# Optimization experiments

Hardware: AMD Instinct MI355X
Metric: run time of the kernel (lower is better)

The kernel has to match this reference:

```python
import jax, jax.numpy as jnp
import numpy as np

NUM_FIELDS = 40
EMBED_DIM = 64
ATTN_DIM = 32

def _triu_index(n):
    i, j = np.triu_indices(n, k=1)
    return jnp.asarray(i, jnp.int32), jnp.asarray(j, jnp.int32)

def setup_inputs() -> dict:
    key = jax.random.key(0)
    k0, k1, k2, k3, k4, k5 = jax.random.split(key, 6)
    B = 8192
    inputs = jax.random.normal(k0, (B, NUM_FIELDS, EMBED_DIM), dtype=jnp.float32)
    # attention MLP params (PyTorch Linear default init scale ~ 1/sqrt(fan_in))
    s1 = 1.0 / np.sqrt(EMBED_DIM)
    s2 = 1.0 / np.sqrt(ATTN_DIM)
    W1 = jax.random.uniform(k1, (EMBED_DIM, ATTN_DIM), jnp.float32, -s1, s1)
    b1 = jax.random.uniform(k2, (ATTN_DIM,), jnp.float32, -s1, s1)
    w2 = jax.random.uniform(k3, (ATTN_DIM,), jnp.float32, -s2, s2)
    p = jax.random.uniform(k4, (EMBED_DIM,), jnp.float32, -s1, s1)
    return {"inputs": inputs, "W1": W1, "b1": b1, "w2": w2, "p": p}

def reference(inputs, W1, b1, w2, p):
    idx0, idx1 = _triu_index(NUM_FIELDS)  # [P], P = 780 pairs
    # gather pairwise field embeddings and take elementwise product: [B, P, D]
    prod = inputs[:, idx0, :] * inputs[:, idx1, :]
    # tiny attention MLP: Linear -> ReLU -> Linear(no bias) -> softmax over pairs
    h = jax.nn.relu(jnp.einsum('bpd,da->bpa', prod, W1) + b1)  # [B, P, A]
    logits = jnp.einsum('bpa,a->bp', h, w2)                    # [B, P]
    attn = jax.nn.softmax(logits, axis=1)                      # softmax over pair dim
    # attention-weighted sum pooling over pairs: [B, D]
    pooled = jnp.einsum('bp,bpd->bd', attn, prod)
    # final linear projection to scalar (dropout=0 / eval -> identity)
    return jnp.einsum('bd,d->b', pooled, p)
```

## Files before the change

### kernel.cpp

```cpp
#include <hip/hip_runtime.h>


typedef _Float16 f16;
typedef f16 f16x2 __attribute__((ext_vector_type(2)));
typedef f16 f16x4 __attribute__((ext_vector_type(4)));
typedef f16 f16x8 __attribute__((ext_vector_type(8)));
typedef float fx16 __attribute__((ext_vector_type(16)));

#define NF 40
#define NB 8192
#define STR 88

union V8 { f16x8 v8; f16x4 v4[2]; f16x2 v2[4]; };

__global__ __launch_bounds__(256, 4) void afm_kernel(
    const float* __restrict__ x,
    const float* __restrict__ W1,
    const float* __restrict__ b1,
    const float* __restrict__ w2,
    const float* __restrict__ p,
    float* __restrict__ out)
{
    __shared__ __align__(16) f16 xh[4][NF * STR];

    const int tid  = threadIdx.x;
    const int wid  = tid >> 6;
    const int lane = tid & 63;
    const int b    = blockIdx.x * 4 + wid;

    f16* Xs = &xh[wid][0];

    const float4* xb = (const float4*)(x + (size_t)b * (NF * 64));
#pragma unroll
    for (int t = 0; t < 5; ++t) {
        int g = t * 64 + lane;
        float4 v0 = xb[g * 2];
        float4 v1 = xb[g * 2 + 1];
        V8 w;
        w.v4[0] = f16x4{ (f16)v0.x, (f16)v0.y, (f16)v0.z, (f16)v0.w };
        w.v4[1] = f16x4{ (f16)v1.x, (f16)v1.y, (f16)v1.z, (f16)v1.w };
        int row = g >> 3, gg = g & 7;
        *(f16x8*)(Xs + row * STR + gg * 8) = w.v8;
    }

    const int nl = lane & 31;
    const int hh = lane >> 5;
    const int h8 = hh * 8;

    f16x8 w1f[4];
#pragma unroll
    for (int kt = 0; kt < 4; ++kt)
#pragma unroll
        for (int j = 0; j < 8; ++j)
            w1f[kt][j] = (f16)W1[(kt * 16 + h8 + j) * 32 + nl];

    f16x2 pp[16];
#pragma unroll
    for (int kt = 0; kt < 4; ++kt)
#pragma unroll
        for (int m = 0; m < 4; ++m) {
            f16x2 t2 = { (f16)p[kt * 16 + h8 + 2 * m], (f16)p[kt * 16 + h8 + 2 * m + 1] };
            pp[kt * 4 + m] = t2;
        }

    fx16 b1C;
    f16x2 w2h[8];
#pragma unroll
    for (int r = 0; r < 16; ++r) {
        int a = (r & 3) + 8 * (r >> 2) + 4 * hh;
        b1C[r] = b1[a];
    }
#pragma unroll
    for (int m = 0; m < 8; ++m) {
        int r = 2 * m;
        int a = (r & 3) + 8 * (r >> 2) + 4 * hh;
        f16x2 t2 = { (f16)(w2[a] * 1.44269504f), (f16)(w2[a + 1] * 1.44269504f) };
        w2h[m] = t2;
    }

    f16x8 xif8[4];
    {
        const f16* src = Xs + nl * STR + h8;
#pragma unroll
        for (int kt = 0; kt < 4; ++kt)
            xif8[kt] = *(const f16x8*)(src + kt * 16);
    }

    float accW = 0.f, accWS = 0.f;

    auto body = [&](const f16x8* xi, int jrow, bool valid) {
        const f16* base = Xs + jrow * STR + h8;
        V8 pr[4];
#pragma unroll
        for (int kt = 0; kt < 4; ++kt) {
            f16x8 xj = *(const f16x8*)(base + kt * 16);
            pr[kt].v8 = xi[kt] * xj;
        }
        fx16 C = __builtin_amdgcn_mfma_f32_32x32x16_f16(w1f[0], pr[0].v8, b1C, 0, 0, 0);
        C = __builtin_amdgcn_mfma_f32_32x32x16_f16(w1f[1], pr[1].v8, C, 0, 0, 0);
        C = __builtin_amdgcn_mfma_f32_32x32x16_f16(w1f[2], pr[2].v8, C, 0, 0, 0);
        C = __builtin_amdgcn_mfma_f32_32x32x16_f16(w1f[3], pr[3].v8, C, 0, 0, 0);
        float s0 = 0.f, s1 = 0.f, s2 = 0.f, s3 = 0.f;
#pragma unroll
        for (int m = 0; m < 4; ++m) {
            s0 = __builtin_amdgcn_fdot2(pr[0].v2[m], pp[m],      s0, false);
            s1 = __builtin_amdgcn_fdot2(pr[1].v2[m], pp[4 + m],  s1, false);
            s2 = __builtin_amdgcn_fdot2(pr[2].v2[m], pp[8 + m],  s2, false);
            s3 = __builtin_amdgcn_fdot2(pr[3].v2[m], pp[12 + m], s3, false);
        }
        float sp = (s0 + s1) + (s2 + s3);
        const f16x2 z2 = { (f16)0.f, (f16)0.f };
        float l0 = 0.f, l1 = 0.f;
#pragma unroll
        for (int m = 0; m < 8; ++m) {
            f16x2 hm = __builtin_bit_cast(f16x2,
                __builtin_amdgcn_cvt_pkrtz(C[2 * m], C[2 * m + 1]));
            hm = __builtin_elementwise_max(hm, z2);
            if (m & 1) l1 = __builtin_amdgcn_fdot2(hm, w2h[m], l1, false);
            else       l0 = __builtin_amdgcn_fdot2(hm, w2h[m], l0, false);
        }
        float l = l0 + l1;
        l += __shfl_xor(l, 32);
        float w = __builtin_amdgcn_exp2f(l);
        if (!valid) w = 0.f;
        accW += w;
        accWS = fmaf(w, sp, accWS);
    };

    for (int t = 1; t <= 24; ++t) {
        int jrow = (t <= 16) ? ((nl + t) & 31) : (t + 15);
        bool valid = (t != 16) || (nl < 16);
        body(xif8, jrow, valid);
    }
    {
        int q = nl < 28 ? nl : 27;
        float disc = 225.0f - 8.0f * (float)q;
        int ii = (int)((15.0f - sqrtf(disc)) * 0.5f);
        if (ii * (15 - ii) / 2 > q) --ii;
        if ((ii + 1) * (14 - ii) / 2 <= q) ++ii;
        int jj = q - ii * (15 - ii) / 2 + ii + 1;
        int iC = 32 + ii, jC = 32 + jj;
        f16x8 xi2[4];
        const f16* src = Xs + iC * STR + h8;
#pragma unroll
        for (int kt = 0; kt < 4; ++kt)
            xi2[kt] = *(const f16x8*)(src + kt * 16);
        body(xi2, jC, nl < 28);
    }

    accWS += __shfl_xor(accWS, 32);
#pragma unroll
    for (int m = 16; m >= 1; m >>= 1) {
        accW  += __shfl_xor(accW, m);
        accWS += __shfl_xor(accWS, m);
    }
    if (lane == 0) out[b] = accWS / accW;
}

extern "C" void kernel_launch(void* const* d_in, const int* in_sizes, int n_in,
                              void* d_out, int out_size, void* d_ws, size_t ws_size,
                              hipStream_t stream) {
    const float* x  = (const float*)d_in[0];
    const float* W1 = (const float*)d_in[1];
    const float* b1 = (const float*)d_in[2];
    const float* w2 = (const float*)d_in[3];
    const float* p  = (const float*)d_in[4];
    float* out = (float*)d_out;
    dim3 grid(NB / 4), block(256);
    hipLaunchKernelGGL(afm_kernel, grid, block, 0, stream, x, W1, b1, w2, p, out);
}
```

Measured before the change: 150.3 us.

## Software-pipeline pair iterations so MFMA of next pair overlaps epilogue of current

Splits the per-pair body into an MFMA/product phase and a ReLU/logit/exp epilogue phase, then double-buffers the accumulators so the next pair's MFMA chain is issued before the previous pair's epilogue. The loop is kept rolled (unroll 1) with two pairs per iteration. Launch bounds are relaxed from 4 to 2 waves per SIMD to give room for the extra 16-float accumulator, which trades occupancy for instruction-level overlap.

```diff
diff --git a/kernel.cpp b/kernel.cpp
--- a/kernel.cpp
+++ b/kernel.cpp
@@ -13,7 +13,50 @@
 
 union V8 { f16x8 v8; f16x4 v4[2]; f16x2 v2[4]; };
 
-__global__ __launch_bounds__(256, 4) void afm_kernel(
+#define AFM_PH1(Cd, spd, XI, JR)                                              \
+    do {                                                                      \
+        const f16* base_ = Xs + (JR) * STR + h8;                              \
+        V8 p0_, p1_, p2_, p3_;                                                \
+        p0_.v8 = (XI)[0] * *(const f16x8*)(base_);          \
+        p1_.v8 = (XI)[1] * *(const f16x8*)(base_ + 16);                       \
+        p2_.v8 = (XI)[2] * *(const f16x8*)(base_ + 32);                       \
+        p3_.v8 = (XI)[3] * *(const f16x8*)(base_ + 48);                       \
+        Cd = __builtin_amdgcn_mfma_f32_32x32x16_f16(w1f[0], p0_.v8, b1C, 0, 0, 0); \
+        Cd = __builtin_amdgcn_mfma_f32_32x32x16_f16(w1f[1], p1_.v8, Cd, 0, 0, 0);  \
+        Cd = __builtin_amdgcn_mfma_f32_32x32x16_f16(w1f[2], p2_.v8, Cd, 0, 0, 0);  \
+        Cd = __builtin_amdgcn_mfma_f32_32x32x16_f16(w1f[3], p3_.v8, Cd, 0, 0, 0);  \
+        float s0_ = 0.f, s1_ = 0.f, s2_ = 0.f, s3_ = 0.f;                     \
+        _Pragma("unroll")                                                     \
+        for (int m_ = 0; m_ < 4; ++m_) {                                      \
+            s0_ = __builtin_amdgcn_fdot2(p0_.v2[m_], pp[m_],      s0_, false);\
+            s1_ = __builtin_amdgcn_fdot2(p1_.v2[m_], pp[4 + m_],  s1_, false);\
+            s2_ = __builtin_amdgcn_fdot2(p2_.v2[m_], pp[8 + m_],  s2_, false);\
+            s3_ = __builtin_amdgcn_fdot2(p3_.v2[m_], pp[12 + m_], s3_, false);\
+        }                                                                     \
+        spd = (s0_ + s1_) + (s2_ + s3_);                                      \
+    } while (0)
+
+#define AFM_PH2(Cs, sps, VOK)                                                 \
+    do {                                                                      \
+        const f16x2 z2_ = { (f16)0.f, (f16)0.f };                             \
+        float l0_ = 0.f, l1_ = 0.f;                                           \
+        _Pragma("unroll")                                                     \
+        for (int m_ = 0; m_ < 8; ++m_) {                                      \
+            f16x2 hm_ = __builtin_bit_cast(f16x2,                             \
+                __builtin_amdgcn_cvt_pkrtz((Cs)[2 * m_], (Cs)[2 * m_ + 1]));  \
+            hm_ = __builtin_elementwise_max(hm_, z2_);      \
+            if (m_ & 1) l1_ = __builtin_amdgcn_fdot2(hm_, w2h[m_], l1_, false);\
+            else        l0_ = __builtin_amdgcn_fdot2(hm_, w2h[m_], l0_, false);\
+        }                                                                     \
+        float l_ = l0_ + l1_;                                                 \
+        l_ += __shfl_xor(l_, 32);                               \
+        float w_ = __builtin_amdgcn_exp2f(l_);               \
+        if (!(VOK)) w_ = 0.f;                                                 \
+        accW += w_;                                                           \
+        accWS = fmaf(w_, sps, accWS);                         \
+    } while (0)
+
+__global__ __launch_bounds__(256, 2) void afm_kernel(
     const float* __restrict__ x,
     const float* __restrict__ W1,
     const float* __restrict__ b1,
@@ -88,50 +131,23 @@
 
     float accW = 0.f, accWS = 0.f;
 
-    auto body = [&](const f16x8* xi, int jrow, bool valid) {
-        const f16* base = Xs + jrow * STR + h8;
-        V8 pr[4];
-#pragma unroll
-        for (int kt = 0; kt < 4; ++kt) {
-            f16x8 xj = *(const f16x8*)(base + kt * 16);
-            pr[kt].v8 = xi[kt] * xj;
-        }
-        fx16 C = __builtin_amdgcn_mfma_f32_32x32x16_f16(w1f[0], pr[0].v8, b1C, 0, 0, 0);
-        C = __builtin_amdgcn_mfma_f32_32x32x16_f16(w1f[1], pr[1].v8, C, 0, 0, 0);
-        C = __builtin_amdgcn_mfma_f32_32x32x16_f16(w1f[2], pr[2].v8, C, 0, 0, 0);
-        C = __builtin_amdgcn_mfma_f32_32x32x16_f16(w1f[3], pr[3].v8, C, 0, 0, 0);
-        float s0 = 0.f, s1 = 0.f, s2 = 0.f, s3 = 0.f;
-#pragma unroll
-        for (int m = 0; m < 4; ++m) {
-            s0 = __builtin_amdgcn_fdot2(pr[0].v2[m], pp[m],      s0, false);
-            s1 = __builtin_amdgcn_fdot2(pr[1].v2[m], pp[4 + m],  s1, false);
-            s2 = __builtin_amdgcn_fdot2(pr[2].v2[m], pp[8 + m],  s2, false);
-            s3 = __builtin_amdgcn_fdot2(pr[3].v2[m], pp[12 + m], s3, false);
-        }
-        float sp = (s0 + s1) + (s2 + s3);
-        const f16x2 z2 = { (f16)0.f, (f16)0.f };
-        float l0 = 0.f, l1 = 0.f;
-#pragma unroll
-        for (int m = 0; m < 8; ++m) {
-            f16x2 hm = __builtin_bit_cast(f16x2,
-                __builtin_amdgcn_cvt_pkrtz(C[2 * m], C[2 * m + 1]));
-            hm = __builtin_elementwise_max(hm, z2);
-            if (m & 1) l1 = __builtin_amdgcn_fdot2(hm, w2h[m], l1, false);
-            else       l0 = __builtin_amdgcn_fdot2(hm, w2h[m], l0, false);
-        }
-        float l = l0 + l1;
-        l += __shfl_xor(l, 32);
-        float w = __builtin_amdgcn_exp2f(l);
-        if (!valid) w = 0.f;
-        accW += w;
-        accWS = fmaf(w, sp, accWS);
-    };
+    fx16 CA, CB;
+    float spA, spB;
+    bool vA, vB;
 
-    for (int t = 1; t <= 24; ++t) {
-        int jrow = (t <= 16) ? ((nl + t) & 31) : (t + 15);
-        bool valid = (t != 16) || (nl < 16);
-        body(xif8, jrow, valid);
+    AFM_PH1(CA, spA, xif8, (nl + 1) & 31); vA = true;
+#pragma unroll 1
+    for (int k = 0; k < 11; ++k) {
+        const int t1 = 2 + 2 * k, t2 = 3 + 2 * k;
+        const int j1 = (t1 <= 16) ? ((nl + t1) & 31) : (t1 + 15);
+        AFM_PH1(CB, spB, xif8, j1); vB = (t1 != 16) || (nl < 16);
+        AFM_PH2(CA, spA, vA);
+        const int j2 = (t2 <= 16) ? ((nl + t2) & 31) : (t2 + 15);
+        AFM_PH1(CA, spA, xif8, j2); vA = (t2 != 16) || (nl < 16);
+        AFM_PH2(CB, spB, vB);
     }
+    AFM_PH1(CB, spB, xif8, 39); vB = true;
+    AFM_PH2(CA, spA, vA);
     {
         int q = nl < 28 ? nl : 27;
         float disc = 225.0f - 8.0f * (float)q;
@@ -145,7 +161,9 @@
 #pragma unroll
         for (int kt = 0; kt < 4; ++kt)
             xi2[kt] = *(const f16x8*)(src + kt * 16);
-        body(xi2, jC, nl < 28);
+        AFM_PH1(CA, spA, xi2, jC); vA = (nl < 28);
+        AFM_PH2(CB, spB, vB);
+        AFM_PH2(CA, spA, vA);
     }
 
     accWS += __shfl_xor(accWS, 32);
```

Measured after the change: 152.4 us. No clear change (+1.4%).
